# Kernel tuning notes

Measured on AMD Instinct MI355X. Metric: run time of the kernel, lower is better.

Reference implementation:

```python
import jax, jax.numpy as jnp
import numpy as np

HEADS = 8

def setup_inputs() -> dict:
    key = jax.random.key(0)
    k1, k2, k3 = jax.random.split(key, 3)
    B, C, L = 8, 512, 4096
    dim_head = 64
    hidden = HEADS * dim_head  # 512
    x = jax.random.normal(k1, (B, C, L), dtype=jnp.float32)
    # Conv1d(dim, hidden*3, 1, bias=False) -> weight [hidden*3, dim]
    w_qkv = jax.random.normal(k2, (hidden * 3, C), dtype=jnp.float32) * 0.02
    # Conv1d(hidden, dim, 1) -> weight [dim, hidden], bias [dim]
    w_out = jax.random.normal(k3, (C, hidden), dtype=jnp.float32) * 0.02
    b_out = jnp.zeros((C,), dtype=jnp.float32)
    return {"x": x, "w_qkv": w_qkv, "w_out": w_out, "b_out": b_out}

def reference(x, w_qkv, w_out, b_out):
    B, C, L = x.shape
    # 1x1 Conv1d == channel matmul
    qkv = jnp.einsum('oc,bcl->bol', w_qkv, x)            # [B, 3*H*dh, L]
    qkv = qkv.reshape(B, 3, HEADS, -1, L)                # qkv outermost, then heads, then c
    q, k, v = qkv[:, 0], qkv[:, 1], qkv[:, 2]            # each [B, H, dh, L]
    k = jax.nn.softmax(k, axis=-1)                       # softmax over sequence
    context = jnp.einsum('bhdn,bhen->bhde', k, v)        # [B, H, dh, dh]
    out = jnp.einsum('bhde,bhdn->bhen', context, q)      # [B, H, dh, L]
    out = out.reshape(B, -1, L)                          # [B, H*dh, L]
    return jnp.einsum('oc,bcl->bol', w_out, out) + b_out[None, :, None]
```

## Files before the change

kernel.cpp:

```cpp
#include <hip/hip_runtime.h>
#include <hip/hip_bf16.h>


typedef __bf16 bf16x8 __attribute__((ext_vector_type(8)));
typedef __bf16 bf16x4 __attribute__((ext_vector_type(4)));
typedef float  f32x4  __attribute__((ext_vector_type(4)));

#define B_  8
#define L_  4096
#define C_  512

#define GLD_LDS16(g, l)                                             \
    __builtin_amdgcn_global_load_lds(                               \
        (const __attribute__((address_space(1))) void*)(g),         \
        (__attribute__((address_space(3))) void*)(l), 16, 0, 0)

#define FENCE asm volatile("" ::: "memory")
#define BAR   do { FENCE; __builtin_amdgcn_s_barrier(); FENCE; } while (0)
#define DRAIN_LGKM asm volatile("s_waitcnt lgkmcnt(0)" ::: "memory")
#define WAIT_VM(N) asm volatile("s_waitcnt vmcnt(" #N ")" ::: "memory")

__global__ __launch_bounds__(256) void prep_all(const float* __restrict__ x,
                                                __hip_bfloat16* __restrict__ xt,
                                                const float* __restrict__ wqkv_f,
                                                __hip_bfloat16* __restrict__ wkv_b,
                                                __hip_bfloat16* __restrict__ wqT) {
    __shared__ float tile[64 * 132];
    int blk = blockIdx.x;
    int t = threadIdx.x;
    if (blk < 2048) {
        int b = blk >> 8, rem = blk & 255;
        int l0 = (rem & 31) * 128, c0 = (rem >> 5) * 64;
        const float* xp = x + ((size_t)b * C_ + c0) * L_ + l0;
#pragma unroll
        for (int p = 0; p < 8; p++) {
            int i = p * 8 + (t >> 5);
            int j = (t & 31) * 4;
            float4 vv = *(const float4*)(xp + (size_t)i * L_ + j);
            *(float4*)&tile[i * 132 + j] = vv;
        }
        __syncthreads();
        unsigned short* xo = (unsigned short*)xt + ((size_t)b * L_ + l0) * C_ + c0;
#pragma unroll
        for (int qq = 0; qq < 8; qq++) {
            int l = qq * 16 + (t >> 4);
            int cg = (t & 15) * 4;
            bf16x4 ov;
#pragma unroll
            for (int k = 0; k < 4; k++) ov[k] = (__bf16)tile[(cg + k) * 132 + l];
            *(bf16x4*)(xo + (size_t)l * C_ + cg) = ov;
        }
    } else if (blk < 4096) {
        int i = (blk - 2048) * 256 + t;
        wkv_b[i] = __float2bfloat16(wqkv_f[512 * 512 + i]);
    } else {
        int tb = blk - 4096;
        int r0 = (tb >> 4) * 32, c0 = (tb & 15) * 32;
        int tx = t & 31, ty = t >> 5;
        for (int r = 0; r < 32; r += 8)
            tile[(ty + r) * 33 + tx] = wqkv_f[(size_t)(r0 + ty + r) * 512 + c0 + tx];
        __syncthreads();
        for (int r = 0; r < 32; r += 8)
            wqT[(size_t)(c0 + ty + r) * 512 + r0 + tx] = __float2bfloat16(tile[tx * 33 + ty + r]);
    }
}

template <int MODE>
__global__ __launch_bounds__(256, 2) void gemm_p(
    const __hip_bfloat16* __restrict__ A, const __hip_bfloat16* __restrict__ Bt,
    size_t strideA, size_t strideB, int M, int N, int K,
    __hip_bfloat16* __restrict__ kb, __hip_bfloat16* __restrict__ vb,
    float* __restrict__ outb, const float* __restrict__ bias) {
    __shared__ alignas(16) unsigned short sA[2][128 * 64];
    __shared__ alignas(16) unsigned short sB[2][128 * 64];

    int b = blockIdx.z;
    int m0 = blockIdx.y * 128, n0 = blockIdx.x * 128;
    const __hip_bfloat16* Ab = A + strideA * (size_t)b;
    const __hip_bfloat16* Bb = Bt + strideB * (size_t)b;

    int t = threadIdx.x;
    int lane = t & 63, wv = t >> 6;
    int l16 = lane & 15, q4 = lane >> 4;
    int wr = (wv >> 1) * 64, wc = (wv & 1) * 64;

    int srow = lane >> 3;
    int swz  = ((lane & 7) ^ srow) * 8;

    const __hip_bfloat16* gA[4];
    const __hip_bfloat16* gB[4];
    unsigned ldoff[4];
#pragma unroll
    for (int c = 0; c < 4; c++) {
        int r = c * 32 + wv * 8;
        gA[c] = Ab + (size_t)(m0 + r + srow) * K + swz;
        gB[c] = Bb + (size_t)(n0 + r + srow) * K + swz;
        ldoff[c] = (unsigned)r * 64;
    }

    int gsel0 = (q4 ^ (l16 & 7)) * 8;
    int gsel1 = gsel0 ^ 32;
    unsigned rA = (unsigned)(wr + l16) * 64;
    unsigned rB = (unsigned)(wc + l16) * 64;
    int NKT = K >> 6;

    f32x4 acc[4][4] = {};
    bf16x8 aF[4][2], bF[4][2];

#pragma unroll
    for (int c = 0; c < 4; c++) GLD_LDS16(gA[c], &sA[0][ldoff[c]]);
#pragma unroll
    for (int c = 0; c < 4; c++) GLD_LDS16(gB[c], &sB[0][ldoff[c]]);
    if (NKT > 1) {
#pragma unroll
        for (int c = 0; c < 4; c++) GLD_LDS16(gA[c] + 64, &sA[1][ldoff[c]]);
        WAIT_VM(4);
    } else {
        WAIT_VM(0);
    }
    BAR;

#pragma unroll 1
    for (int kt = 0; kt < NKT; ++kt) {
        int cur = kt & 1, nbuf = cur ^ 1;
        const unsigned short* As_b = sA[cur];
        const unsigned short* Bs_b = sB[cur];
        bool st1 = (kt + 1) < NKT;
        bool st2 = (kt + 2) < NKT;

#pragma unroll
        for (int i = 0; i < 4; i++) {
            aF[i][0] = *(const bf16x8*)&As_b[rA + i * 1024 + gsel0];
            aF[i][1] = *(const bf16x8*)&As_b[rA + i * 1024 + gsel1];
        }
#pragma unroll
        for (int j = 0; j < 2; j++) {
            bF[j][0] = *(const bf16x8*)&Bs_b[rB + j * 1024 + gsel0];
            bF[j][1] = *(const bf16x8*)&Bs_b[rB + j * 1024 + gsel1];
        }
        if (st1) {
            int ko = (kt + 1) << 6;
#pragma unroll
            for (int c = 0; c < 4; c++) GLD_LDS16(gB[c] + ko, &sB[nbuf][ldoff[c]]);
        }
        BAR;
        __builtin_amdgcn_s_setprio(1);
#pragma unroll
        for (int ks = 0; ks < 2; ks++)
#pragma unroll
            for (int i = 0; i < 4; i++)
#pragma unroll
                for (int j = 0; j < 2; j++)
                    acc[i][j] = __builtin_amdgcn_mfma_f32_16x16x32_bf16(aF[i][ks], bF[j][ks], acc[i][j], 0, 0, 0);
        __builtin_amdgcn_s_setprio(0);
        DRAIN_LGKM;
        BAR;

#pragma unroll
        for (int j = 2; j < 4; j++) {
            bF[j][0] = *(const bf16x8*)&Bs_b[rB + j * 1024 + gsel0];
            bF[j][1] = *(const bf16x8*)&Bs_b[rB + j * 1024 + gsel1];
        }
        if (st2) {
            int ko = (kt + 2) << 6;
#pragma unroll
            for (int c = 0; c < 4; c++) GLD_LDS16(gA[c] + ko, &sA[cur][ldoff[c]]);
        }
        BAR;
        __builtin_amdgcn_s_setprio(1);
#pragma unroll
        for (int ks = 0; ks < 2; ks++)
#pragma unroll
            for (int i = 0; i < 4; i++)
#pragma unroll
                for (int j = 0; j < 2; j++)
                    acc[i][2 + j] = __builtin_amdgcn_mfma_f32_16x16x32_bf16(aF[i][ks], bF[2 + j][ks], acc[i][2 + j], 0, 0, 0);
        __builtin_amdgcn_s_setprio(0);
        DRAIN_LGKM;
        if (st2) { WAIT_VM(4); } else { WAIT_VM(0); }
        BAR;
    }

#pragma unroll
    for (int i = 0; i < 4; i++)
#pragma unroll
        for (int j = 0; j < 4; j++)
#pragma unroll
            for (int r = 0; r < 4; r++) {
                int row = m0 + wr + i * 16 + q4 * 4 + r;
                int col = n0 + wc + j * 16 + l16;
                float val = acc[i][j][r];
                if (MODE == 1) {
                    __hip_bfloat16* dst = (m0 < 512) ? kb : vb;
                    int od = row & 511;
                    dst[((size_t)b * 512 + od) * (size_t)N + col] = __float2bfloat16(val);
                } else {
                    outb[((size_t)b * M + row) * (size_t)N + col] = val + bias[row];
                }
            }
}

template <int MODE>
__global__ __launch_bounds__(256) void gemm_bt(
    const __hip_bfloat16* __restrict__ A, const __hip_bfloat16* __restrict__ Bt,
    size_t strideA, size_t strideB, int M, int N, int K,
    __hip_bfloat16* __restrict__ obf) {
    __shared__ alignas(16) unsigned short As[128 * 64];
    __shared__ alignas(16) unsigned short Bs[128 * 64];

    int b = blockIdx.z;
    int m0 = blockIdx.y * 128, n0 = blockIdx.x * 128;
    const __hip_bfloat16* Ab = A + strideA * (size_t)b;
    const __hip_bfloat16* Bb = Bt + strideB * (size_t)b;

    int t = threadIdx.x;
    int lane = t & 63, wv = t >> 6;
    int l16 = lane & 15, q4 = lane >> 4;
    int wr = (wv >> 1) * 64, wc = (wv & 1) * 64;

    int srow = lane >> 3;
    int swz  = ((lane & 7) ^ srow) * 8;

    const __hip_bfloat16* gA[4];
    const __hip_bfloat16* gB[4];
    unsigned short* lA[4];
    unsigned short* lB[4];
#pragma unroll
    for (int c = 0; c < 4; c++) {
        int r = wv * 32 + c * 8;
        gA[c] = Ab + (size_t)(m0 + r + srow) * K + swz;
        gB[c] = Bb + (size_t)(n0 + r + srow) * K + swz;
        lA[c] = &As[r * 64];
        lB[c] = &Bs[r * 64];
    }

    int gsel0 = ((q4) ^ (l16 & 7)) * 8;
    int gsel1 = gsel0 ^ 32;
    int rA = (wr + l16) * 64;
    int rB = (wc + l16) * 64;

    f32x4 acc[4][4] = {};

    for (int k0 = 0; k0 < K; k0 += 64) {
        __syncthreads();
#pragma unroll
        for (int c = 0; c < 4; c++) {
            GLD_LDS16(gA[c] + k0, lA[c]);
            GLD_LDS16(gB[c] + k0, lB[c]);
        }
        __syncthreads();

        bf16x8 af[4], bfr[4];
#pragma unroll
        for (int i = 0; i < 4; i++) {
            af[i]  = *(const bf16x8*)&As[rA + i * 1024 + gsel0];
            bfr[i] = *(const bf16x8*)&Bs[rB + i * 1024 + gsel0];
        }
#pragma unroll
        for (int i = 0; i < 4; i++)
#pragma unroll
            for (int j = 0; j < 4; j++)
                acc[i][j] = __builtin_amdgcn_mfma_f32_16x16x32_bf16(af[i], bfr[j], acc[i][j], 0, 0, 0);
#pragma unroll
        for (int i = 0; i < 4; i++) {
            af[i]  = *(const bf16x8*)&As[rA + i * 1024 + gsel1];
            bfr[i] = *(const bf16x8*)&Bs[rB + i * 1024 + gsel1];
        }
#pragma unroll
        for (int i = 0; i < 4; i++)
#pragma unroll
            for (int j = 0; j < 4; j++)
                acc[i][j] = __builtin_amdgcn_mfma_f32_16x16x32_bf16(af[i], bfr[j], acc[i][j], 0, 0, 0);
    }

#pragma unroll
    for (int i = 0; i < 4; i++)
#pragma unroll
        for (int j = 0; j < 4; j++)
#pragma unroll
            for (int r = 0; r < 4; r++) {
                int row = m0 + wr + i * 16 + q4 * 4 + r;
                int col = n0 + wc + j * 16 + l16;
                obf[((size_t)b * 512 + row) * (size_t)N + col] = __float2bfloat16(acc[i][j][r]);
            }
}

__global__ __launch_bounds__(256) void ctx_kernel(const __hip_bfloat16* __restrict__ kraw,
                                                  const __hip_bfloat16* __restrict__ v,
                                                  float* __restrict__ ctxp,
                                                  float* __restrict__ sums) {
    int kc = blockIdx.x, h = blockIdx.y, b = blockIdx.z;
    int t = threadIdx.x, lane = t & 63, wv = t >> 6;
    int l16 = lane & 15, q4 = lane >> 4;
    const __hip_bfloat16* ka = kraw + ((size_t)b * 512 + h * 64) * L_;
    const __hip_bfloat16* va = v + ((size_t)b * 512 + h * 64) * L_;

    f32x4 acc[4][4] = {};
    float ps[4] = {0.f, 0.f, 0.f, 0.f};
    int nbase = kc * 1024 + wv * 256;
#pragma unroll 1
    for (int s = 0; s < 8; s++) {
        int n = nbase + s * 32 + q4 * 8;
        bf16x8 af[4], bfr[4];
#pragma unroll
        for (int i = 0; i < 4; i++) {
            bf16x8 kv = *(const bf16x8*)(ka + (size_t)(i * 16 + l16) * L_ + n);
#pragma unroll
            for (int e = 0; e < 8; e++) {
                float ev = __expf((float)kv[e]);
                af[i][e] = (__bf16)ev;
                ps[i] += ev;
            }
            bfr[i] = *(const bf16x8*)(va + (size_t)(i * 16 + l16) * L_ + n);
        }
#pragma unroll
        for (int i = 0; i < 4; i++)
#pragma unroll
            for (int j = 0; j < 4; j++)
                acc[i][j] = __builtin_amdgcn_mfma_f32_16x16x32_bf16(af[i], bfr[j], acc[i][j], 0, 0, 0);
    }

    __shared__ float sred[4][64];
#pragma unroll
    for (int i = 0; i < 4; i++) {
        ps[i] += __shfl_xor(ps[i], 16, 64);
        ps[i] += __shfl_xor(ps[i], 32, 64);
    }
    if (q4 == 0) {
#pragma unroll
        for (int i = 0; i < 4; i++) sred[wv][i * 16 + l16] = ps[i];
    }
    __syncthreads();
    if (t < 64) {
        float S = sred[0][t] + sred[1][t] + sred[2][t] + sred[3][t];
        sums[(((size_t)kc * 8 + b) * 8 + h) * 64 + t] = S;
    }

    __shared__ float cbuf[4096];
    for (int w = 0; w < 4; w++) {
        if (wv == w) {
#pragma unroll
            for (int i = 0; i < 4; i++)
#pragma unroll
                for (int j = 0; j < 4; j++)
#pragma unroll
                    for (int r = 0; r < 4; r++) {
                        int mm = i * 16 + q4 * 4 + r, nn = j * 16 + l16;
                        float pv = acc[i][j][r];
                        if (w == 0) cbuf[mm * 64 + nn] = pv;
                        else        cbuf[mm * 64 + nn] += pv;
                    }
        }
        __syncthreads();
    }
    float* cg = ctxp + (((size_t)kc * 8 + b) * 8 + h) * 4096;
    for (int i = t; i < 4096; i += 256) cg[i] = cbuf[i];
}

__global__ __launch_bounds__(256) void w2_kernel(const float* __restrict__ wout,
                                                 const float* __restrict__ ctxp,
                                                 const float* __restrict__ sums,
                                                 __hip_bfloat16* __restrict__ w2) {
    int ob = blockIdx.x, h = blockIdx.y, b = blockIdx.z;
    __shared__ float cT[64 * 65];
    __shared__ float wT[64 * 65];
    __shared__ float Sinv[64];
    int t = threadIdx.x;
    const size_t KCS = (size_t)8 * 8 * 4096;
    const float* cg = ctxp + (((size_t)b) * 8 + h) * 4096;
    for (int i = t; i < 4096; i += 256) {
        int d = i >> 6, e = i & 63;
        float s = cg[i] + cg[KCS + i] + cg[2 * KCS + i] + cg[3 * KCS + i];
        cT[e * 65 + d] = s;
        wT[e * 65 + d] = wout[(size_t)(ob * 64 + d) * 512 + h * 64 + e];
    }
    if (t < 64) {
        const size_t SKC = (size_t)8 * 8 * 64;
        const float* sg = sums + ((size_t)b * 8 + h) * 64;
        float S = sg[t] + sg[SKC + t] + sg[2 * SKC + t] + sg[3 * SKC + t];
        Sinv[t] = 1.0f / S;
    }
    __syncthreads();
    int ol = t >> 2;
    int db = (t & 3) * 16;
    for (int dd = 0; dd < 16; dd++) {
        int d = db + dd;
        float s = 0.f;
#pragma unroll
        for (int e = 0; e < 64; e++) s += wT[e * 65 + ol] * cT[e * 65 + d];
        w2[((size_t)b * 512 + ob * 64 + ol) * 512 + h * 64 + d] = __float2bfloat16(s * Sinv[d]);
    }
}

extern "C" void kernel_launch(void* const* d_in, const int* in_sizes, int n_in,
                              void* d_out, int out_size, void* d_ws, size_t ws_size,
                              hipStream_t stream) {
    const float* x     = (const float*)d_in[0];
    const float* w_qkv = (const float*)d_in[1];
    const float* w_out = (const float*)d_in[2];
    const float* b_out = (const float*)d_in[3];
    float* out = (float*)d_out;
    char* ws = (char*)d_ws;

    const size_t QKV = (size_t)B_ * 512 * L_;
    size_t off_xt   = 0;
    size_t off_wkv  = off_xt + (size_t)B_ * L_ * C_ * 2;
    size_t off_wqT  = off_wkv + (size_t)1024 * 512 * 2;
    size_t off_k    = off_wqT + (size_t)512 * 512 * 2;
    size_t off_v    = off_k + QKV * 2;
    size_t off_ctxp = off_v + QKV * 2;
    size_t off_sums = off_ctxp + (size_t)4 * 8 * 8 * 4096 * 4;
    size_t off_w2   = off_k;
    size_t off_w3   = off_k + (size_t)B_ * 512 * 512 * 2;

    __hip_bfloat16* xt   = (__hip_bfloat16*)(ws + off_xt);
    __hip_bfloat16* wkvb = (__hip_bfloat16*)(ws + off_wkv);
    __hip_bfloat16* wqT  = (__hip_bfloat16*)(ws + off_wqT);
    __hip_bfloat16* kb   = (__hip_bfloat16*)(ws + off_k);
    __hip_bfloat16* vb   = (__hip_bfloat16*)(ws + off_v);
    float*          ctxp = (float*)(ws + off_ctxp);
    float*          sums = (float*)(ws + off_sums);
    __hip_bfloat16* w2   = (__hip_bfloat16*)(ws + off_w2);
    __hip_bfloat16* W3   = (__hip_bfloat16*)(ws + off_w3);

    prep_all<<<4352, 256, 0, stream>>>(x, xt, w_qkv, wkvb, wqT);

    gemm_p<1><<<dim3(L_ / 128, 1024 / 128, B_), 256, 0, stream>>>(
        wkvb, xt, 0, (size_t)L_ * C_, 1024, L_, 512, kb, vb, nullptr, nullptr);

    ctx_kernel<<<dim3(4, 8, B_), 256, 0, stream>>>(kb, vb, ctxp, sums);

    w2_kernel<<<dim3(8, 8, B_), 256, 0, stream>>>(w_out, ctxp, sums, w2);

    gemm_bt<3><<<dim3(512 / 128, 512 / 128, B_), 256, 0, stream>>>(
        w2, wqT, (size_t)512 * 512, 0, 512, 512, 512, W3);

    gemm_p<2><<<dim3(L_ / 128, 512 / 128, B_), 256, 0, stream>>>(
        W3, xt, (size_t)512 * 512, (size_t)L_ * C_, 512, L_, 512, nullptr, nullptr, out, b_out);
}
```

Before: 244.4 us.

## Fuse K/V projection with softmax-exp and context accumulation via atomics

The K/V projection GEMM now computes a per-head 64-row K tile and 64-row V tile for each 128-column chunk of the sequence. In its epilogue it exponentiates K, writes P and V to shared memory, and runs a small MFMA to produce partial context. Partial context and row sums are accumulated into global memory with atomicAdd, so the bf16 K/V intermediates and the separate ctx_kernel are no longer needed. This removes a large round-trip of K/V through global memory. In exchange it adds heavy atomic contention (32 blocks per head add into the same 4096 context entries) and a zeroing pass folded into the prep kernel. The softmax normalisation moves into w2_kernel, which also gets a 4-wide vectorised inner loop and store.

Result: no change. 245.5 us (+0.5%).

```diff
diff --git a/kernel.cpp b/kernel.cpp
--- a/kernel.cpp
+++ b/kernel.cpp
@@ -24,7 +24,8 @@
                                                 __hip_bfloat16* __restrict__ xt,
                                                 const float* __restrict__ wqkv_f,
                                                 __hip_bfloat16* __restrict__ wkv_b,
-                                                __hip_bfloat16* __restrict__ wqT) {
+                                                __hip_bfloat16* __restrict__ wqT,
+                                                float* __restrict__ zero_base) {
     __shared__ float tile[64 * 132];
     int blk = blockIdx.x;
     int t = threadIdx.x;
@@ -53,7 +54,7 @@
     } else if (blk < 4096) {
         int i = (blk - 2048) * 256 + t;
         wkv_b[i] = __float2bfloat16(wqkv_f[512 * 512 + i]);
-    } else {
+    } else if (blk < 4352) {
         int tb = blk - 4096;
         int r0 = (tb >> 4) * 32, c0 = (tb & 15) * 32;
         int tx = t & 31, ty = t >> 5;
@@ -62,22 +63,22 @@
         __syncthreads();
         for (int r = 0; r < 32; r += 8)
             wqT[(size_t)(c0 + ty + r) * 512 + r0 + tx] = __float2bfloat16(tile[tx * 33 + ty + r]);
+    } else {
+        int i = (blk - 4352) * 256 + t;
+        zero_base[i] = 0.f;
     }
 }
 
-template <int MODE>
-__global__ __launch_bounds__(256, 2) void gemm_p(
+__global__ __launch_bounds__(256, 2) void gemm_kv(
     const __hip_bfloat16* __restrict__ A, const __hip_bfloat16* __restrict__ Bt,
-    size_t strideA, size_t strideB, int M, int N, int K,
-    __hip_bfloat16* __restrict__ kb, __hip_bfloat16* __restrict__ vb,
-    float* __restrict__ outb, const float* __restrict__ bias) {
+    float* __restrict__ ctx, float* __restrict__ Ssum) {
     __shared__ alignas(16) unsigned short sA[2][128 * 64];
     __shared__ alignas(16) unsigned short sB[2][128 * 64];
 
-    int b = blockIdx.z;
-    int m0 = blockIdx.y * 128, n0 = blockIdx.x * 128;
-    const __hip_bfloat16* Ab = A + strideA * (size_t)b;
-    const __hip_bfloat16* Bb = Bt + strideB * (size_t)b;
+    const int K = C_;
+    int b = blockIdx.z, h = blockIdx.y;
+    int n0 = blockIdx.x * 128;
+    const __hip_bfloat16* Bb = Bt + (size_t)b * L_ * C_;
 
     int t = threadIdx.x;
     int lane = t & 63, wv = t >> 6;
@@ -93,8 +94,10 @@
 #pragma unroll
     for (int c = 0; c < 4; c++) {
         int r = c * 32 + wv * 8;
-        gA[c] = Ab + (size_t)(m0 + r + srow) * K + swz;
-        gB[c] = Bb + (size_t)(n0 + r + srow) * K + swz;
+        int lr = r + srow;
+        int grow = h * 64 + lr + (lr >= 64 ? 448 : 0);
+        gA[c] = A + (size_t)grow * K + swz;
+        gB[c] = Bb + (size_t)(n0 + lr) * K + swz;
         ldoff[c] = (unsigned)r * 64;
     }
 
@@ -102,7 +105,7 @@
     int gsel1 = gsel0 ^ 32;
     unsigned rA = (unsigned)(wr + l16) * 64;
     unsigned rB = (unsigned)(wc + l16) * 64;
-    int NKT = K >> 6;
+    const int NKT = K >> 6;
 
     f32x4 acc[4][4] = {};
     bf16x8 aF[4][2], bF[4][2];
@@ -111,13 +114,9 @@
     for (int c = 0; c < 4; c++) GLD_LDS16(gA[c], &sA[0][ldoff[c]]);
 #pragma unroll
     for (int c = 0; c < 4; c++) GLD_LDS16(gB[c], &sB[0][ldoff[c]]);
-    if (NKT > 1) {
-#pragma unroll
-        for (int c = 0; c < 4; c++) GLD_LDS16(gA[c] + 64, &sA[1][ldoff[c]]);
-        WAIT_VM(4);
-    } else {
-        WAIT_VM(0);
-    }
+#pragma unroll
+    for (int c = 0; c < 4; c++) GLD_LDS16(gA[c] + 64, &sA[1][ldoff[c]]);
+    WAIT_VM(4);
     BAR;
 
 #pragma unroll 1
@@ -181,6 +180,181 @@
         BAR;
     }
 
+    __bf16* Pb = (__bf16*)sA;
+    __bf16* Vb = (__bf16*)sB;
+    float* ctxg = ctx  + ((size_t)b * 8 + h) * 4096;
+    float* Sg   = Ssum + ((size_t)b * 8 + h) * 64;
+
+    if (wv < 2) {
+#pragma unroll
+        for (int i = 0; i < 4; i++)
+#pragma unroll
+            for (int r = 0; r < 4; r++) {
+                int d = i * 16 + q4 * 4 + r;
+                float rs = 0.f;
+#pragma unroll
+                for (int j = 0; j < 4; j++) {
+                    int n = wc + j * 16 + l16;
+                    float pv = __expf(acc[i][j][r]);
+                    rs += pv;
+                    Pb[d * 128 + (((n >> 3) ^ (d & 15)) * 8) + (n & 7)] = (__bf16)pv;
+                }
+                rs += __shfl_xor(rs, 1, 64);
+                rs += __shfl_xor(rs, 2, 64);
+                rs += __shfl_xor(rs, 4, 64);
+                rs += __shfl_xor(rs, 8, 64);
+                if (l16 == 0) atomicAdd(&Sg[d], rs);
+            }
+    } else {
+#pragma unroll
+        for (int i = 0; i < 4; i++)
+#pragma unroll
+            for (int j = 0; j < 4; j++)
+#pragma unroll
+                for (int r = 0; r < 4; r++) {
+                    int e = i * 16 + q4 * 4 + r;
+                    int n = wc + j * 16 + l16;
+                    Vb[e * 128 + (((n >> 3) ^ (e & 15)) * 8) + (n & 7)] = (__bf16)acc[i][j][r];
+                }
+    }
+    DRAIN_LGKM;
+    BAR;
+
+    f32x4 acc2[4] = {};
+#pragma unroll
+    for (int kk = 0; kk < 4; kk++) {
+        int gg = kk * 4 + q4;
+        bf16x8 bf2 = *(const bf16x8*)&Vb[(wv * 16 + l16) * 128 + ((gg ^ l16) * 8)];
+#pragma unroll
+        for (int i2 = 0; i2 < 4; i2++) {
+            bf16x8 af2 = *(const bf16x8*)&Pb[(i2 * 16 + l16) * 128 + ((gg ^ l16) * 8)];
+            acc2[i2] = __builtin_amdgcn_mfma_f32_16x16x32_bf16(af2, bf2, acc2[i2], 0, 0, 0);
+        }
+    }
+#pragma unroll
+    for (int i2 = 0; i2 < 4; i2++)
+#pragma unroll
+        for (int r = 0; r < 4; r++) {
+            int d = i2 * 16 + q4 * 4 + r;
+            int e = wv * 16 + l16;
+            atomicAdd(&ctxg[d * 64 + e], acc2[i2][r]);
+        }
+}
+
+__global__ __launch_bounds__(256, 2) void gemm_p(
+    const __hip_bfloat16* __restrict__ A, const __hip_bfloat16* __restrict__ Bt,
+    size_t strideA, size_t strideB, int M, int N, int K,
+    float* __restrict__ outb, const float* __restrict__ bias) {
+    __shared__ alignas(16) unsigned short sA[2][128 * 64];
+    __shared__ alignas(16) unsigned short sB[2][128 * 64];
+
+    int b = blockIdx.z;
+    int m0 = blockIdx.y * 128, n0 = blockIdx.x * 128;
+    const __hip_bfloat16* Ab = A + strideA * (size_t)b;
+    const __hip_bfloat16* Bb = Bt + strideB * (size_t)b;
+
+    int t = threadIdx.x;
+    int lane = t & 63, wv = t >> 6;
+    int l16 = lane & 15, q4 = lane >> 4;
+    int wr = (wv >> 1) * 64, wc = (wv & 1) * 64;
+
+    int srow = lane >> 3;
+    int swz  = ((lane & 7) ^ srow) * 8;
+
+    const __hip_bfloat16* gA[4];
+    const __hip_bfloat16* gB[4];
+    unsigned ldoff[4];
+#pragma unroll
+    for (int c = 0; c < 4; c++) {
+        int r = c * 32 + wv * 8;
+        gA[c] = Ab + (size_t)(m0 + r + srow) * K + swz;
+        gB[c] = Bb + (size_t)(n0 + r + srow) * K + swz;
+        ldoff[c] = (unsigned)r * 64;
+    }
+
+    int gsel0 = (q4 ^ (l16 & 7)) * 8;
+    int gsel1 = gsel0 ^ 32;
+    unsigned rA = (unsigned)(wr + l16) * 64;
+    unsigned rB = (unsigned)(wc + l16) * 64;
+    int NKT = K >> 6;
+
+    f32x4 acc[4][4] = {};
+    bf16x8 aF[4][2], bF[4][2];
+
+#pragma unroll
+    for (int c = 0; c < 4; c++) GLD_LDS16(gA[c], &sA[0][ldoff[c]]);
+#pragma unroll
+    for (int c = 0; c < 4; c++) GLD_LDS16(gB[c], &sB[0][ldoff[c]]);
+    if (NKT > 1) {
+#pragma unroll
+        for (int c = 0; c < 4; c++) GLD_LDS16(gA[c] + 64, &sA[1][ldoff[c]]);
+        WAIT_VM(4);
+    } else {
+        WAIT_VM(0);
+    }
+    BAR;
+
+#pragma unroll 1
+    for (int kt = 0; kt < NKT; ++kt) {
+        int cur = kt & 1, nbuf = cur ^ 1;
+        const unsigned short* As_b = sA[cur];
+        const unsigned short* Bs_b = sB[cur];
+        bool st1 = (kt + 1) < NKT;
+        bool st2 = (kt + 2) < NKT;
+
+#pragma unroll
+        for (int i = 0; i < 4; i++) {
+            aF[i][0] = *(const bf16x8*)&As_b[rA + i * 1024 + gsel0];
+            aF[i][1] = *(const bf16x8*)&As_b[rA + i * 1024 + gsel1];
+        }
+#pragma unroll
+        for (int j = 0; j < 2; j++) {
+            bF[j][0] = *(const bf16x8*)&Bs_b[rB + j * 1024 + gsel0];
+            bF[j][1] = *(const bf16x8*)&Bs_b[rB + j * 1024 + gsel1];
+        }
+        if (st1) {
+            int ko = (kt + 1) << 6;
+#pragma unroll
+            for (int c = 0; c < 4; c++) GLD_LDS16(gB[c] + ko, &sB[nbuf][ldoff[c]]);
+        }
+        BAR;
+        __builtin_amdgcn_s_setprio(1);
+#pragma unroll
+        for (int ks = 0; ks < 2; ks++)
+#pragma unroll
+            for (int i = 0; i < 4; i++)
+#pragma unroll
+                for (int j = 0; j < 2; j++)
+                    acc[i][j] = __builtin_amdgcn_mfma_f32_16x16x32_bf16(aF[i][ks], bF[j][ks], acc[i][j], 0, 0, 0);
+        __builtin_amdgcn_s_setprio(0);
+        DRAIN_LGKM;
+        BAR;
+
+#pragma unroll
+        for (int j = 2; j < 4; j++) {
+            bF[j][0] = *(const bf16x8*)&Bs_b[rB + j * 1024 + gsel0];
+            bF[j][1] = *(const bf16x8*)&Bs_b[rB + j * 1024 + gsel1];
+        }
+        if (st2) {
+            int ko = (kt + 2) << 6;
+#pragma unroll
+            for (int c = 0; c < 4; c++) GLD_LDS16(gA[c] + ko, &sA[cur][ldoff[c]]);
+        }
+        BAR;
+        __builtin_amdgcn_s_setprio(1);
+#pragma unroll
+        for (int ks = 0; ks < 2; ks++)
+#pragma unroll
+            for (int i = 0; i < 4; i++)
+#pragma unroll
+                for (int j = 0; j < 2; j++)
+                    acc[i][2 + j] = __builtin_amdgcn_mfma_f32_16x16x32_bf16(aF[i][ks], bF[2 + j][ks], acc[i][2 + j], 0, 0, 0);
+        __builtin_amdgcn_s_setprio(0);
+        DRAIN_LGKM;
+        if (st2) { WAIT_VM(4); } else { WAIT_VM(0); }
+        BAR;
+    }
+
 #pragma unroll
     for (int i = 0; i < 4; i++)
 #pragma unroll
@@ -189,18 +363,10 @@
             for (int r = 0; r < 4; r++) {
                 int row = m0 + wr + i * 16 + q4 * 4 + r;
                 int col = n0 + wc + j * 16 + l16;
-                float val = acc[i][j][r];
-                if (MODE == 1) {
-                    __hip_bfloat16* dst = (m0 < 512) ? kb : vb;
-                    int od = row & 511;
-                    dst[((size_t)b * 512 + od) * (size_t)N + col] = __float2bfloat16(val);
-                } else {
-                    outb[((size_t)b * M + row) * (size_t)N + col] = val + bias[row];
-                }
+                outb[((size_t)b * M + row) * (size_t)N + col] = acc[i][j][r] + bias[row];
             }
 }
 
-template <int MODE>
 __global__ __launch_bounds__(256) void gemm_bt(
     const __hip_bfloat16* __restrict__ A, const __hip_bfloat16* __restrict__ Bt,
     size_t strideA, size_t strideB, int M, int N, int K,
@@ -285,110 +451,41 @@
             }
 }
 
-__global__ __launch_bounds__(256) void ctx_kernel(const __hip_bfloat16* __restrict__ kraw,
-                                                  const __hip_bfloat16* __restrict__ v,
-                                                  float* __restrict__ ctxp,
-                                                  float* __restrict__ sums) {
-    int kc = blockIdx.x, h = blockIdx.y, b = blockIdx.z;
-    int t = threadIdx.x, lane = t & 63, wv = t >> 6;
-    int l16 = lane & 15, q4 = lane >> 4;
-    const __hip_bfloat16* ka = kraw + ((size_t)b * 512 + h * 64) * L_;
-    const __hip_bfloat16* va = v + ((size_t)b * 512 + h * 64) * L_;
-
-    f32x4 acc[4][4] = {};
-    float ps[4] = {0.f, 0.f, 0.f, 0.f};
-    int nbase = kc * 1024 + wv * 256;
-#pragma unroll 1
-    for (int s = 0; s < 8; s++) {
-        int n = nbase + s * 32 + q4 * 8;
-        bf16x8 af[4], bfr[4];
-#pragma unroll
-        for (int i = 0; i < 4; i++) {
-            bf16x8 kv = *(const bf16x8*)(ka + (size_t)(i * 16 + l16) * L_ + n);
-#pragma unroll
-            for (int e = 0; e < 8; e++) {
-                float ev = __expf((float)kv[e]);
-                af[i][e] = (__bf16)ev;
-                ps[i] += ev;
-            }
-            bfr[i] = *(const bf16x8*)(va + (size_t)(i * 16 + l16) * L_ + n);
-        }
-#pragma unroll
-        for (int i = 0; i < 4; i++)
-#pragma unroll
-            for (int j = 0; j < 4; j++)
-                acc[i][j] = __builtin_amdgcn_mfma_f32_16x16x32_bf16(af[i], bfr[j], acc[i][j], 0, 0, 0);
-    }
-
-    __shared__ float sred[4][64];
-#pragma unroll
-    for (int i = 0; i < 4; i++) {
-        ps[i] += __shfl_xor(ps[i], 16, 64);
-        ps[i] += __shfl_xor(ps[i], 32, 64);
-    }
-    if (q4 == 0) {
-#pragma unroll
-        for (int i = 0; i < 4; i++) sred[wv][i * 16 + l16] = ps[i];
-    }
-    __syncthreads();
-    if (t < 64) {
-        float S = sred[0][t] + sred[1][t] + sred[2][t] + sred[3][t];
-        sums[(((size_t)kc * 8 + b) * 8 + h) * 64 + t] = S;
-    }
-
-    __shared__ float cbuf[4096];
-    for (int w = 0; w < 4; w++) {
-        if (wv == w) {
-#pragma unroll
-            for (int i = 0; i < 4; i++)
-#pragma unroll
-                for (int j = 0; j < 4; j++)
-#pragma unroll
-                    for (int r = 0; r < 4; r++) {
-                        int mm = i * 16 + q4 * 4 + r, nn = j * 16 + l16;
-                        float pv = acc[i][j][r];
-                        if (w == 0) cbuf[mm * 64 + nn] = pv;
-                        else        cbuf[mm * 64 + nn] += pv;
-                    }
-        }
-        __syncthreads();
-    }
-    float* cg = ctxp + (((size_t)kc * 8 + b) * 8 + h) * 4096;
-    for (int i = t; i < 4096; i += 256) cg[i] = cbuf[i];
-}
-
 __global__ __launch_bounds__(256) void w2_kernel(const float* __restrict__ wout,
-                                                 const float* __restrict__ ctxp,
-                                                 const float* __restrict__ sums,
+                                                 const float* __restrict__ ctx,
+                                                 const float* __restrict__ Ssum,
                                                  __hip_bfloat16* __restrict__ w2) {
     int ob = blockIdx.x, h = blockIdx.y, b = blockIdx.z;
     __shared__ float cT[64 * 65];
     __shared__ float wT[64 * 65];
     __shared__ float Sinv[64];
     int t = threadIdx.x;
-    const size_t KCS = (size_t)8 * 8 * 4096;
-    const float* cg = ctxp + (((size_t)b) * 8 + h) * 4096;
+    const float* cg = ctx + ((size_t)b * 8 + h) * 4096;
+    if (t < 64) Sinv[t] = 1.0f / Ssum[((size_t)b * 8 + h) * 64 + t];
+    __syncthreads();
     for (int i = t; i < 4096; i += 256) {
         int d = i >> 6, e = i & 63;
-        float s = cg[i] + cg[KCS + i] + cg[2 * KCS + i] + cg[3 * KCS + i];
-        cT[e * 65 + d] = s;
+        cT[e * 65 + d] = cg[i] * Sinv[d];
         wT[e * 65 + d] = wout[(size_t)(ob * 64 + d) * 512 + h * 64 + e];
-    }
-    if (t < 64) {
-        const size_t SKC = (size_t)8 * 8 * 64;
-        const float* sg = sums + ((size_t)b * 8 + h) * 64;
-        float S = sg[t] + sg[SKC + t] + sg[2 * SKC + t] + sg[3 * SKC + t];
-        Sinv[t] = 1.0f / S;
     }
     __syncthreads();
     int ol = t >> 2;
     int db = (t & 3) * 16;
-    for (int dd = 0; dd < 16; dd++) {
-        int d = db + dd;
-        float s = 0.f;
-#pragma unroll
-        for (int e = 0; e < 64; e++) s += wT[e * 65 + ol] * cT[e * 65 + d];
-        w2[((size_t)b * 512 + ob * 64 + ol) * 512 + h * 64 + d] = __float2bfloat16(s * Sinv[d]);
+    unsigned short* w2p = (unsigned short*)w2 + ((size_t)b * 512 + ob * 64 + ol) * 512 + h * 64;
+    for (int g = 0; g < 4; g++) {
+        int d0 = db + g * 4;
+        float s0 = 0.f, s1 = 0.f, s2 = 0.f, s3 = 0.f;
+#pragma unroll
+        for (int e = 0; e < 64; e++) {
+            float w = wT[e * 65 + ol];
+            s0 += w * cT[e * 65 + d0];
+            s1 += w * cT[e * 65 + d0 + 1];
+            s2 += w * cT[e * 65 + d0 + 2];
+            s3 += w * cT[e * 65 + d0 + 3];
+        }
+        bf16x4 ov;
+        ov[0] = (__bf16)s0; ov[1] = (__bf16)s1; ov[2] = (__bf16)s2; ov[3] = (__bf16)s3;
+        *(bf16x4*)(w2p + d0) = ov;
     }
 }
 
@@ -402,39 +499,31 @@
     float* out = (float*)d_out;
     char* ws = (char*)d_ws;
 
-    const size_t QKV = (size_t)B_ * 512 * L_;
-    size_t off_xt   = 0;
-    size_t off_wkv  = off_xt + (size_t)B_ * L_ * C_ * 2;
-    size_t off_wqT  = off_wkv + (size_t)1024 * 512 * 2;
-    size_t off_k    = off_wqT + (size_t)512 * 512 * 2;
-    size_t off_v    = off_k + QKV * 2;
-    size_t off_ctxp = off_v + QKV * 2;
-    size_t off_sums = off_ctxp + (size_t)4 * 8 * 8 * 4096 * 4;
-    size_t off_w2   = off_k;
-    size_t off_w3   = off_k + (size_t)B_ * 512 * 512 * 2;
+    size_t off_xt  = 0;
+    size_t off_wkv = off_xt + (size_t)B_ * L_ * C_ * 2;
+    size_t off_wqT = off_wkv + (size_t)1024 * 512 * 2;
+    size_t off_ctx = off_wqT + (size_t)512 * 512 * 2;
+    size_t off_S   = off_ctx + (size_t)B_ * 8 * 4096 * 4;
+    size_t off_w2  = off_S + (size_t)B_ * 8 * 64 * 4;
+    size_t off_w3  = off_w2 + (size_t)B_ * 512 * 512 * 2;
 
     __hip_bfloat16* xt   = (__hip_bfloat16*)(ws + off_xt);
     __hip_bfloat16* wkvb = (__hip_bfloat16*)(ws + off_wkv);
     __hip_bfloat16* wqT  = (__hip_bfloat16*)(ws + off_wqT);
-    __hip_bfloat16* kb   = (__hip_bfloat16*)(ws + off_k);
-    __hip_bfloat16* vb   = (__hip_bfloat16*)(ws + off_v);
-    float*          ctxp = (float*)(ws + off_ctxp);
-    float*          sums = (float*)(ws + off_sums);
+    float*          ctx  = (float*)(ws + off_ctx);
+    float*          Sv   = (float*)(ws + off_S);
     __hip_bfloat16* w2   = (__hip_bfloat16*)(ws + off_w2);
     __hip_bfloat16* W3   = (__hip_bfloat16*)(ws + off_w3);
 
-    prep_all<<<4352, 256, 0, stream>>>(x, xt, w_qkv, wkvb, wqT);
-
-    gemm_p<1><<<dim3(L_ / 128, 1024 / 128, B_), 256, 0, stream>>>(
-        wkvb, xt, 0, (size_t)L_ * C_, 1024, L_, 512, kb, vb, nullptr, nullptr);
-
-    ctx_kernel<<<dim3(4, 8, B_), 256, 0, stream>>>(kb, vb, ctxp, sums);
-
-    w2_kernel<<<dim3(8, 8, B_), 256, 0, stream>>>(w_out, ctxp, sums, w2);
-
-    gemm_bt<3><<<dim3(512 / 128, 512 / 128, B_), 256, 0, stream>>>(
+    prep_all<<<5392, 256, 0, stream>>>(x, xt, w_qkv, wkvb, wqT, ctx);
+
+    gemm_kv<<<dim3(L_ / 128, 8, B_), 256, 0, stream>>>(wkvb, xt, ctx, Sv);
+
+    w2_kernel<<<dim3(8, 8, B_), 256, 0, stream>>>(w_out, ctx, Sv, w2);
+
+    gemm_bt<<<dim3(512 / 128, 512 / 128, B_), 256, 0, stream>>>(
         w2, wqT, (size_t)512 * 512, 0, 512, 512, 512, W3);
 
-    gemm_p<2><<<dim3(L_ / 128, 512 / 128, B_), 256, 0, stream>>>(
-        W3, xt, (size_t)512 * 512, (size_t)L_ * C_, 512, L_, 512, nullptr, nullptr, out, b_out);
+    gemm_p<<<dim3(L_ / 128, 512 / 128, B_), 256, 0, stream>>>(
+        W3, xt, (size_t)512 * 512, (size_t)L_ * C_, 512, L_, 512, out, b_out);
 }
```
